# Optimization experiments

Hardware: AMD Instinct MI355X
Metric: run time of the kernel (lower is better)

The kernel has to match this reference:

```python
import jax, jax.numpy as jnp
import numpy as np

E, N, D_IN, HID, TD, H = 800000, 50000, 64, 32, 32, 4
HO = H * HID
VOCAB = 1000000


def time_encode(t, dim):
    # t: [E,1] -> [E,dim], interleaved sin/cos harmonic encoding
    div_term = jnp.exp(jnp.arange(0, dim, 2, dtype=jnp.float32) * (-jnp.log(10000.0) / dim))
    ang = t * div_term  # [E, dim//2]
    return jnp.stack([jnp.sin(ang), jnp.cos(ang)], axis=-1).reshape(t.shape[0], dim)


def tgat_conv(x, src, dst, t_feat, wq, bq, wk, bk, wv, bv, wt, bt, num_nodes):
    # x: [N, Fin]; t_feat: [E, TD]
    q = (x @ wq + bq).reshape(-1, H, HID)
    k = (x @ wk + bk).reshape(-1, H, HID)
    v = (x @ wv + bv).reshape(-1, H, HID)
    te = (t_feat @ wt + bt).reshape(-1, H, HID)
    q_i = q[dst]                      # [E,H,HID] gather at target
    k_j = k[src] + te                 # [E,H,HID] gather at source + time enc
    alpha = jnp.sum(q_i * k_j, axis=-1) / jnp.sqrt(jnp.float32(HID))  # [E,H]
    # segment softmax over edges grouped by destination node
    m = jax.ops.segment_max(alpha, dst, num_segments=num_nodes)        # [N,H]
    ex = jnp.exp(alpha - m[dst])
    s = jax.ops.segment_sum(ex, dst, num_segments=num_nodes)           # [N,H]
    a = ex / (s[dst] + 1e-16)                                          # [E,H]
    msg = v[src] * a[:, :, None]                                       # [E,H,HID]
    out = jax.ops.segment_sum(msg, dst, num_segments=num_nodes)        # [N,H,HID]
    return out.reshape(num_nodes, HO)


def setup_inputs() -> dict:
    key = jax.random.key(0)
    ks = jax.random.split(key, 24)

    def lin_w(k, fi, fo):
        return jax.random.normal(k, (fi, fo), dtype=jnp.float32) / jnp.sqrt(jnp.float32(fi))

    inp = {
        'edge_index': jax.random.randint(ks[0], (2, E), 0, N),
        'edge_attr': jax.random.uniform(ks[1], (E, 2), dtype=jnp.float32),
        'num_nodes': N,
        'emb': jax.random.normal(ks[2], (VOCAB, D_IN), dtype=jnp.float32) * 0.1,
        'wq1': lin_w(ks[3], D_IN, HO), 'bq1': jnp.zeros((HO,), jnp.float32),
        'wk1': lin_w(ks[4], D_IN, HO), 'bk1': jnp.zeros((HO,), jnp.float32),
        'wv1': lin_w(ks[5], D_IN, HO), 'bv1': jnp.zeros((HO,), jnp.float32),
        'wt1': lin_w(ks[6], TD, HO), 'bt1': jnp.zeros((HO,), jnp.float32),
        'wq2': lin_w(ks[7], HO, HO), 'bq2': jnp.zeros((HO,), jnp.float32),
        'wk2': lin_w(ks[8], HO, HO), 'bk2': jnp.zeros((HO,), jnp.float32),
        'wv2': lin_w(ks[9], HO, HO), 'bv2': jnp.zeros((HO,), jnp.float32),
        'wt2': lin_w(ks[10], TD, HO), 'bt2': jnp.zeros((HO,), jnp.float32),
        'wc': lin_w(ks[11], HO, 1), 'bc': jnp.zeros((1,), jnp.float32),
    }
    return inp


def reference(edge_index, edge_attr, num_nodes, emb,
              wq1, bq1, wk1, bk1, wv1, bv1, wt1, bt1,
              wq2, bq2, wk2, bk2, wv2, bv2, wt2, bt2,
              wc, bc):
    src, dst = edge_index[0], edge_index[1]
    x = emb[:num_nodes]                                   # node_emb(arange(N))
    raw_time = edge_attr[:, 1:2]                          # [E,1]
    t_feat = time_encode(raw_time, TD)                    # [E,TD]
    x = jax.nn.relu(tgat_conv(x, src, dst, t_feat, wq1, bq1, wk1, bk1, wv1, bv1, wt1, bt1, num_nodes))
    x = jax.nn.relu(tgat_conv(x, src, dst, t_feat, wq2, bq2, wk2, bk2, wv2, bv2, wt2, bt2, num_nodes))
    edge_emb = x[src] + x[dst]                            # [E,HO]
    return (edge_emb @ wc + bc).squeeze(-1)               # [E]
```

## Files before the change

### kernel.cpp

```cpp
#include <hip/hip_runtime.h>
#include <hip/hip_bf16.h>

#define NNODES 50000
#define HOUT   128
#define NHEAD  4
#define HID    32
#define TDIM   32

typedef _Float16 h8 __attribute__((ext_vector_type(8)));

__constant__ float DIVT[16] = {
    1.0f, 0.5623413251903491f, 0.31622776601683794f, 0.1778279410038923f,
    0.1f, 0.05623413251903491f, 0.03162277660168379f, 0.01778279410038923f,
    0.01f, 0.005623413251903491f, 0.003162277660168379f, 0.001778279410038923f,
    0.001f, 0.0005623413251903491f, 0.0003162277660168379f, 0.0001778279410038923f
};

__global__ __launch_bounds__(128) void prep_wqt_kernel(
    const float* __restrict__ wq, const float* __restrict__ bq,
    const float* __restrict__ wt, float* __restrict__ wqt,
    float* __restrict__ bqt, int din)
{
    __shared__ float wts[TDIM * HOUT];
    const int tid = threadIdx.x;
    for (int i = tid; i < TDIM * HOUT; i += 128) wts[i] = wt[i];
    __syncthreads();
    const int h = tid >> 5;
    const int t = tid & 31;
    const int d = blockIdx.x;
    const float* row = (d == din) ? bq : wq + (size_t)d * HOUT;
    float s = 0.f;
    #pragma unroll
    for (int d2 = 0; d2 < 32; d2++)
        s += row[h * 32 + d2] * wts[t * HOUT + h * 32 + d2];
    if (d == din) bqt[h * 32 + t] = s;
    else          wqt[(size_t)d * HOUT + h * 32 + t] = s;
}

__global__ __launch_bounds__(256) void gemm_qkv_kernel(
    const float* __restrict__ X, int din, int n,
    const float* __restrict__ W0, const float* __restrict__ W1,
    const float* __restrict__ W2, const float* __restrict__ W3,
    const float* __restrict__ B0, const float* __restrict__ B1,
    const float* __restrict__ B2, const float* __restrict__ B3,
    float* __restrict__ q, _Float16* __restrict__ kv, float* __restrict__ qwt)
{
    const int y = blockIdx.y;
    const float* W = (y == 0) ? W0 : (y == 1) ? W1 : (y == 2) ? W2 : W3;
    const float* B = (y == 0) ? B0 : (y == 1) ? B1 : (y == 2) ? B2 : B3;

    __shared__ float Xs[64 * 68];
    __shared__ float Ws[64 * HOUT];

    const int tid  = threadIdx.x;
    const int row0 = blockIdx.x * 64;
    const int rg   = tid >> 4;
    const int cg   = tid & 15;

    float acc[4][8];
    #pragma unroll
    for (int r = 0; r < 4; r++)
        #pragma unroll
        for (int c = 0; c < 8; c++) acc[r][c] = 0.f;

    const int ktiles = din >> 6;
    for (int kt = 0; kt < ktiles; kt++) {
        {
            const int lrow = tid >> 2;
            const int k0   = (tid & 3) << 4;
            const int grow = row0 + lrow;
            const float* src = X + (size_t)grow * din + kt * 64 + k0;
            #pragma unroll
            for (int i = 0; i < 4; i++) {
                float4 val = (grow < n) ? ((const float4*)src)[i]
                                        : make_float4(0.f, 0.f, 0.f, 0.f);
                *(float4*)&Xs[lrow * 68 + k0 + i * 4] = val;
            }
        }
        {
            const int k  = tid >> 2;
            const int c0 = (tid & 3) << 5;
            const float* src = W + (size_t)(kt * 64 + k) * HOUT + c0;
            #pragma unroll
            for (int i = 0; i < 8; i++)
                *(float4*)&Ws[k * HOUT + c0 + i * 4] = ((const float4*)src)[i];
        }
        __syncthreads();

        #pragma unroll 8
        for (int k = 0; k < 64; k++) {
            float4 b0 = *(const float4*)&Ws[k * HOUT + cg * 8];
            float4 b1 = *(const float4*)&Ws[k * HOUT + cg * 8 + 4];
            #pragma unroll
            for (int r = 0; r < 4; r++) {
                float a = Xs[(rg * 4 + r) * 68 + k];
                acc[r][0] += a * b0.x; acc[r][1] += a * b0.y;
                acc[r][2] += a * b0.z; acc[r][3] += a * b0.w;
                acc[r][4] += a * b1.x; acc[r][5] += a * b1.y;
                acc[r][6] += a * b1.z; acc[r][7] += a * b1.w;
            }
        }
        __syncthreads();
    }

    float4 bb0 = *(const float4*)&B[cg * 8];
    float4 bb1 = *(const float4*)&B[cg * 8 + 4];
    #pragma unroll
    for (int r = 0; r < 4; r++) {
        const int grow = row0 + rg * 4 + r;
        if (grow >= n) continue;
        float o[8] = {acc[r][0] + bb0.x, acc[r][1] + bb0.y, acc[r][2] + bb0.z,
                      acc[r][3] + bb0.w, acc[r][4] + bb1.x, acc[r][5] + bb1.y,
                      acc[r][6] + bb1.z, acc[r][7] + bb1.w};
        if (y == 0 || y == 3) {
            float* O = (y == 0) ? q : qwt;
            *(float4*)&O[(size_t)grow * HOUT + cg * 8]     = make_float4(o[0], o[1], o[2], o[3]);
            *(float4*)&O[(size_t)grow * HOUT + cg * 8 + 4] = make_float4(o[4], o[5], o[6], o[7]);
        } else {
            _Float16* O = kv + ((y == 1) ? 0 : 128);
            h8 hv;
            #pragma unroll
            for (int j = 0; j < 8; j++) hv[j] = (_Float16)o[j];
            *(h8*)&O[(size_t)grow * 256 + cg * 8] = hv;
        }
    }
}

__global__ __launch_bounds__(256) void hist_kernel(
    const int* __restrict__ ei, int* __restrict__ cnt, int E)
{
    const int e = blockIdx.x * 256 + threadIdx.x;
    if (e >= E) return;
    atomicAdd(&cnt[ei[E + e]], 1);
}

__global__ __launch_bounds__(1024) void scan_kernel(
    const int* __restrict__ cnt, int* __restrict__ off, int n)
{
    __shared__ int wsum[16];
    const int tid   = threadIdx.x;
    const int chunk = (n + 1023) >> 10;
    const int lo    = min(tid * chunk, n);
    const int hi    = min(lo + chunk, n);
    int s = 0;
    for (int i = lo; i < hi; i++) s += cnt[i];

    const int lane = tid & 63, wv = tid >> 6;
    int v = s;
    #pragma unroll
    for (int d = 1; d < 64; d <<= 1) {
        int t = __shfl_up(v, d);
        if (lane >= d) v += t;
    }
    if (lane == 63) wsum[wv] = v;
    __syncthreads();
    if (wv == 0 && lane < 16) {
        int w = wsum[lane];
        #pragma unroll
        for (int d = 1; d < 16; d <<= 1) {
            int t = __shfl_up(w, d);
            if (lane >= d) w += t;
        }
        wsum[lane] = w;
    }
    __syncthreads();
    int run = ((wv > 0) ? wsum[wv - 1] : 0) + (v - s);
    for (int i = lo; i < hi; i++) { off[i] = run; run += cnt[i]; }
    if (tid == 1023) off[n] = run;
}

__global__ __launch_bounds__(256) void scatter_kernel(
    const int* __restrict__ ei, const float* __restrict__ ea,
    const int* __restrict__ off, int* __restrict__ cur,
    int2* __restrict__ recs, int E)
{
    const int e = blockIdx.x * 256 + threadIdx.x;
    if (e >= E) return;
    const int dn = ei[E + e];
    const int pos = off[dn] + atomicAdd(&cur[dn], 1);
    recs[pos] = make_int2(ei[e], __float_as_int(ea[2 * e + 1]));
}

__global__ __launch_bounds__(256) void node_attn_kernel(
    const int* __restrict__ off, const int2* __restrict__ recs,
    const float* __restrict__ q, const _Float16* __restrict__ kv,
    const float* __restrict__ qwt, const float* __restrict__ bt,
    float* __restrict__ x, const float* __restrict__ wc,
    float* __restrict__ p, int n)
{
    const int wid = (blockIdx.x * 256 + threadIdx.x) >> 6;
    if (wid >= n) return;
    const int lane = threadIdx.x & 63;
    const int slot = lane >> 4;
    const int sub  = lane & 15;
    const int c0   = sub * 8;
    const int dn   = wid;

    const float4* qv = (const float4*)(q   + (size_t)dn * HOUT + c0);
    const float4* wv = (const float4*)(qwt + (size_t)dn * HOUT + c0);
    const float4 q0 = qv[0], q1 = qv[1];
    const float4 w0 = wv[0], w1 = wv[1];

    const float4 bt0 = ((const float4*)(bt + c0))[0];
    const float4 bt1 = ((const float4*)(bt + c0))[1];
    float qb = q0.x * bt0.x + q0.y * bt0.y + q0.z * bt0.z + q0.w * bt0.w +
               q1.x * bt1.x + q1.y * bt1.y + q1.z * bt1.z + q1.w * bt1.w;
    qb += __shfl_xor(qb, 1);
    qb += __shfl_xor(qb, 2);

    const int beg = off[dn];
    const int end = off[dn + 1];

    float acc[8] = {0.f, 0.f, 0.f, 0.f, 0.f, 0.f, 0.f, 0.f};
    float den = 0.f;

    for (int i = beg + slot; i < end; i += 4) {
        const int2 rec = recs[i];
        const int   sn = rec.x;
        const float rt = __int_as_float(rec.y);

        const h8 kk = *(const h8*)(kv + (size_t)sn * 256 + c0);
        const h8 vv = *(const h8*)(kv + (size_t)sn * 256 + 128 + c0);

        const int i0 = (sub & 3) * 4;
        float tf[8];
        #pragma unroll
        for (int jj = 0; jj < 4; jj++) {
            float s_, c_;
            __sincosf(rt * DIVT[i0 + jj], &s_, &c_);
            tf[2 * jj]     = s_;
            tf[2 * jj + 1] = c_;
        }

        float partial =
            q0.x * (float)kk[0] + q0.y * (float)kk[1] +
            q0.z * (float)kk[2] + q0.w * (float)kk[3] +
            q1.x * (float)kk[4] + q1.y * (float)kk[5] +
            q1.z * (float)kk[6] + q1.w * (float)kk[7] +
            w0.x * tf[0] + w0.y * tf[1] + w0.z * tf[2] + w0.w * tf[3] +
            w1.x * tf[4] + w1.y * tf[5] + w1.z * tf[6] + w1.w * tf[7];
        if ((sub & 3) == 0) partial += qb;

        partial += __shfl_xor(partial, 1);
        partial += __shfl_xor(partial, 2);

        const float ex = __expf(partial * 0.17677669529663687f);
        den += ex;
        #pragma unroll
        for (int j = 0; j < 8; j++) acc[j] += ex * (float)vv[j];
    }

    #pragma unroll
    for (int j = 0; j < 8; j++) {
        acc[j] += __shfl_xor(acc[j], 16);
        acc[j] += __shfl_xor(acc[j], 32);
    }
    den += __shfl_xor(den, 16);
    den += __shfl_xor(den, 32);

    if (lane < 16) {
        const float inv = 1.f / (den + 1e-16f);
        float o[8];
        #pragma unroll
        for (int j = 0; j < 8; j++) o[j] = fmaxf(acc[j] * inv, 0.f);
        if (p == nullptr) {
            float* xo = x + (size_t)dn * HOUT + c0;
            *(float4*)xo       = make_float4(o[0], o[1], o[2], o[3]);
            *((float4*)xo + 1) = make_float4(o[4], o[5], o[6], o[7]);
        } else {
            const float4 wc0 = ((const float4*)(wc + c0))[0];
            const float4 wc1 = ((const float4*)(wc + c0))[1];
            float pp = o[0] * wc0.x + o[1] * wc0.y + o[2] * wc0.z + o[3] * wc0.w +
                       o[4] * wc1.x + o[5] * wc1.y + o[6] * wc1.z + o[7] * wc1.w;
            pp += __shfl_xor(pp, 1);
            pp += __shfl_xor(pp, 2);
            pp += __shfl_xor(pp, 4);
            pp += __shfl_xor(pp, 8);
            if (sub == 0) p[dn] = pp;
        }
    }
}

__global__ __launch_bounds__(256) void edge_out_kernel(
    const int* __restrict__ ei, const float* __restrict__ p,
    const float* __restrict__ bc, float* __restrict__ out, int E)
{
    const int e = blockIdx.x * 256 + threadIdx.x;
    if (e >= E) return;
    out[e] = p[ei[e]] + p[ei[E + e]] + bc[0];
}

extern "C" void kernel_launch(void* const* d_in, const int* in_sizes, int n_in,
                              void* d_out, int out_size, void* d_ws, size_t ws_size,
                              hipStream_t stream)
{
    const int E = in_sizes[0] / 2;
    const int N = NNODES;

    const int*   ei  = (const int*)d_in[0];
    const float* ea  = (const float*)d_in[1];
    const float* emb = (const float*)d_in[3];
    const float *wq1 = (const float*)d_in[4],  *bq1 = (const float*)d_in[5];
    const float *wk1 = (const float*)d_in[6],  *bk1 = (const float*)d_in[7];
    const float *wv1 = (const float*)d_in[8],  *bv1 = (const float*)d_in[9];
    const float *wt1 = (const float*)d_in[10], *bt1 = (const float*)d_in[11];
    const float *wq2 = (const float*)d_in[12], *bq2 = (const float*)d_in[13];
    const float *wk2 = (const float*)d_in[14], *bk2 = (const float*)d_in[15];
    const float *wv2 = (const float*)d_in[16], *bv2 = (const float*)d_in[17];
    const float *wt2 = (const float*)d_in[18], *bt2 = (const float*)d_in[19];
    const float *wc  = (const float*)d_in[20], *bc  = (const float*)d_in[21];
    float* out = (float*)d_out;

    float* ws = (float*)d_ws;
    const size_t NF = (size_t)N * HOUT;
    float*     q    = ws;
    float*     qwt  = ws + NF;
    float*     xbuf = ws + 2 * NF;
    _Float16*  kv   = (_Float16*)(ws + 3 * NF);
    int2*      recs = (int2*)(ws + 4 * NF);
    float*     wqt1 = (float*)(recs + E);
    float*     wqt2 = wqt1 + 64 * HOUT;
    float*     bqt1 = wqt2 + 128 * HOUT;
    float*     bqt2 = bqt1 + HOUT;
    int*       cnt  = (int*)(bqt2 + HOUT);
    int*       off  = cnt + N;
    int*       cur  = off + N + 1;
    float*     p    = (float*)(cur + N);

    const dim3 ggemm((N + 63) / 64, 4);
    const int  eblk = (E + 255) / 256;
    const int  nblk = (N + 3) / 4;

    prep_wqt_kernel<<<65, 128, 0, stream>>>(wq1, bq1, wt1, wqt1, bqt1, 64);
    prep_wqt_kernel<<<129, 128, 0, stream>>>(wq2, bq2, wt2, wqt2, bqt2, 128);

    hipMemsetAsync(cnt, 0, (size_t)N * sizeof(int), stream);
    hipMemsetAsync(cur, 0, (size_t)N * sizeof(int), stream);
    hist_kernel<<<eblk, 256, 0, stream>>>(ei, cnt, E);
    scan_kernel<<<1, 1024, 0, stream>>>(cnt, off, N);
    scatter_kernel<<<eblk, 256, 0, stream>>>(ei, ea, off, cur, recs, E);

    gemm_qkv_kernel<<<ggemm, 256, 0, stream>>>(emb, 64, N,
        wq1, wk1, wv1, wqt1, bq1, bk1, bv1, bqt1, q, kv, qwt);
    node_attn_kernel<<<nblk, 256, 0, stream>>>(off, recs, q, kv, qwt, bt1,
                                               xbuf, nullptr, nullptr, N);

    gemm_qkv_kernel<<<ggemm, 256, 0, stream>>>(xbuf, 128, N,
        wq2, wk2, wv2, wqt2, bq2, bk2, bv2, bqt2, q, kv, qwt);
    node_attn_kernel<<<nblk, 256, 0, stream>>>(off, recs, q, kv, qwt, bt2,
                                               nullptr, wc, p, N);

    edge_out_kernel<<<(E + 255) / 256, 256, 0, stream>>>(ei, p, bc, out, E);
}
```

Before: 772.4 us.

## Use split-fp16 MFMA for QKV projection GEMM and parallelize offset scan

Replaces the scalar FP32 QKV GEMM with MFMA 16x16x32 f16 instructions. Inputs and weights are split into hi and lo halves (three MFMAs per tile) to keep near-FP32 accuracy, and a new prep kernel pre-splits and transposes the weights. Separately, the single-block serial CSR offset scan becomes a three-kernel multi-block scan over int4 chunks. These target the compute cost of the projection GEMMs and the serial scan latency. In exchange they add extra launches, more shared-memory traffic, and scalar (non-vectorized) output stores.

```diff
diff --git a/kernel.cpp b/kernel.cpp
--- a/kernel.cpp
+++ b/kernel.cpp
@@ -8,6 +8,8 @@
 #define TDIM   32
 
 typedef _Float16 h8 __attribute__((ext_vector_type(8)));
+typedef _Float16 h4 __attribute__((ext_vector_type(4)));
+typedef float    f4 __attribute__((ext_vector_type(4)));
 
 __constant__ float DIVT[16] = {
     1.0f, 0.5623413251903491f, 0.31622776601683794f, 0.1778279410038923f,
@@ -37,31 +39,53 @@
     else          wqt[(size_t)d * HOUT + h * 32 + t] = s;
 }
 
-__global__ __launch_bounds__(256) void gemm_qkv_kernel(
-    const float* __restrict__ X, int din, int n,
+__global__ void prep_wsplit_kernel(
     const float* __restrict__ W0, const float* __restrict__ W1,
     const float* __restrict__ W2, const float* __restrict__ W3,
+    _Float16* __restrict__ hi, _Float16* __restrict__ lo, int din)
+{
+    const int y = blockIdx.y, col = blockIdx.x, k = threadIdx.x;
+    const float* W = (y == 0) ? W0 : (y == 1) ? W1 : (y == 2) ? W2 : W3;
+    const float w = W[(size_t)k * HOUT + col];
+    const _Float16 h = (_Float16)w;
+    const size_t idx = ((size_t)y * HOUT + col) * din + k;
+    hi[idx] = h;
+    lo[idx] = (_Float16)(w - (float)h);
+}
+
+#define GPITCH 72
+
+__global__ __launch_bounds__(256) void gemm_qkv_mfma_kernel(
+    const float* __restrict__ X, int din, int n,
+    const _Float16* __restrict__ Whi, const _Float16* __restrict__ Wlo,
     const float* __restrict__ B0, const float* __restrict__ B1,
     const float* __restrict__ B2, const float* __restrict__ B3,
     float* __restrict__ q, _Float16* __restrict__ kv, float* __restrict__ qwt)
 {
     const int y = blockIdx.y;
-    const float* W = (y == 0) ? W0 : (y == 1) ? W1 : (y == 2) ? W2 : W3;
     const float* B = (y == 0) ? B0 : (y == 1) ? B1 : (y == 2) ? B2 : B3;
-
-    __shared__ float Xs[64 * 68];
-    __shared__ float Ws[64 * HOUT];
+    const _Float16* Wy_hi = Whi + (size_t)y * HOUT * din;
+    const _Float16* Wy_lo = Wlo + (size_t)y * HOUT * din;
+
+    __shared__ _Float16 Xh[64 * GPITCH];
+    __shared__ _Float16 Xl[64 * GPITCH];
+    __shared__ _Float16 Bh[128 * GPITCH];
+    __shared__ _Float16 Bl[128 * GPITCH];
 
     const int tid  = threadIdx.x;
     const int row0 = blockIdx.x * 64;
-    const int rg   = tid >> 4;
-    const int cg   = tid & 15;
-
-    float acc[4][8];
-    #pragma unroll
-    for (int r = 0; r < 4; r++)
-        #pragma unroll
-        for (int c = 0; c < 8; c++) acc[r][c] = 0.f;
+    const int wv   = tid >> 6;
+    const int lane = tid & 63;
+    const int lm   = lane & 15;
+    const int g    = lane >> 4;
+
+    f4 acc[8];
+    #pragma unroll
+    for (int ct = 0; ct < 8; ct++) acc[ct] = (f4){0.f, 0.f, 0.f, 0.f};
+
+    float bias[8];
+    #pragma unroll
+    for (int ct = 0; ct < 8; ct++) bias[ct] = B[ct * 16 + lm];
 
     const int ktiles = din >> 6;
     for (int kt = 0; kt < ktiles; kt++) {
@@ -72,56 +96,60 @@
             const float* src = X + (size_t)grow * din + kt * 64 + k0;
             #pragma unroll
             for (int i = 0; i < 4; i++) {
-                float4 val = (grow < n) ? ((const float4*)src)[i]
-                                        : make_float4(0.f, 0.f, 0.f, 0.f);
-                *(float4*)&Xs[lrow * 68 + k0 + i * 4] = val;
+                float4 v = (grow < n) ? ((const float4*)src)[i]
+                                      : make_float4(0.f, 0.f, 0.f, 0.f);
+                h4 hi, lo;
+                hi[0] = (_Float16)v.x; hi[1] = (_Float16)v.y;
+                hi[2] = (_Float16)v.z; hi[3] = (_Float16)v.w;
+                lo[0] = (_Float16)(v.x - (float)hi[0]);
+                lo[1] = (_Float16)(v.y - (float)hi[1]);
+                lo[2] = (_Float16)(v.z - (float)hi[2]);
+                lo[3] = (_Float16)(v.w - (float)hi[3]);
+                *(h4*)&Xh[lrow * GPITCH + k0 + 4 * i] = hi;
+                *(h4*)&Xl[lrow * GPITCH + k0 + 4 * i] = lo;
             }
         }
         {
-            const int k  = tid >> 2;
-            const int c0 = (tid & 3) << 5;
-            const float* src = W + (size_t)(kt * 64 + k) * HOUT + c0;
+            const int col = tid >> 1;
+            const int kk0 = (tid & 1) << 5;
+            const _Float16* sh = Wy_hi + (size_t)col * din + kt * 64 + kk0;
+            const _Float16* sl = Wy_lo + (size_t)col * din + kt * 64 + kk0;
             #pragma unroll
-            for (int i = 0; i < 8; i++)
-                *(float4*)&Ws[k * HOUT + c0 + i * 4] = ((const float4*)src)[i];
+            for (int i = 0; i < 4; i++) {
+                *(h8*)&Bh[col * GPITCH + kk0 + 8 * i] = ((const h8*)sh)[i];
+                *(h8*)&Bl[col * GPITCH + kk0 + 8 * i] = ((const h8*)sl)[i];
+            }
         }
         __syncthreads();
 
-        #pragma unroll 8
-        for (int k = 0; k < 64; k++) {
-            float4 b0 = *(const float4*)&Ws[k * HOUT + cg * 8];
-            float4 b1 = *(const float4*)&Ws[k * HOUT + cg * 8 + 4];
+        #pragma unroll
+        for (int kc = 0; kc < 2; kc++) {
+            const int kb = kc * 32 + g * 8;
+            const h8 ah = *(const h8*)&Xh[(wv * 16 + lm) * GPITCH + kb];
+            const h8 al = *(const h8*)&Xl[(wv * 16 + lm) * GPITCH + kb];
             #pragma unroll
-            for (int r = 0; r < 4; r++) {
-                float a = Xs[(rg * 4 + r) * 68 + k];
-                acc[r][0] += a * b0.x; acc[r][1] += a * b0.y;
-                acc[r][2] += a * b0.z; acc[r][3] += a * b0.w;
-                acc[r][4] += a * b1.x; acc[r][5] += a * b1.y;
-                acc[r][6] += a * b1.z; acc[r][7] += a * b1.w;
+            for (int ct = 0; ct < 8; ct++) {
+                const h8 bh = *(const h8*)&Bh[(ct * 16 + lm) * GPITCH + kb];
+                const h8 bl = *(const h8*)&Bl[(ct * 16 + lm) * GPITCH + kb];
+                acc[ct] = __builtin_amdgcn_mfma_f32_16x16x32_f16(ah, bh, acc[ct], 0, 0, 0);
+                acc[ct] = __builtin_amdgcn_mfma_f32_16x16x32_f16(al, bh, acc[ct], 0, 0, 0);
+                acc[ct] = __builtin_amdgcn_mfma_f32_16x16x32_f16(ah, bl, acc[ct], 0, 0, 0);
             }
         }
         __syncthreads();
     }
 
-    float4 bb0 = *(const float4*)&B[cg * 8];
-    float4 bb1 = *(const float4*)&B[cg * 8 + 4];
-    #pragma unroll
-    for (int r = 0; r < 4; r++) {
-        const int grow = row0 + rg * 4 + r;
-        if (grow >= n) continue;
-        float o[8] = {acc[r][0] + bb0.x, acc[r][1] + bb0.y, acc[r][2] + bb0.z,
-                      acc[r][3] + bb0.w, acc[r][4] + bb1.x, acc[r][5] + bb1.y,
-                      acc[r][6] + bb1.z, acc[r][7] + bb1.w};
-        if (y == 0 || y == 3) {
-            float* O = (y == 0) ? q : qwt;
-            *(float4*)&O[(size_t)grow * HOUT + cg * 8]     = make_float4(o[0], o[1], o[2], o[3]);
-            *(float4*)&O[(size_t)grow * HOUT + cg * 8 + 4] = make_float4(o[4], o[5], o[6], o[7]);
-        } else {
-            _Float16* O = kv + ((y == 1) ? 0 : 128);
-            h8 hv;
-            #pragma unroll
-            for (int j = 0; j < 8; j++) hv[j] = (_Float16)o[j];
-            *(h8*)&O[(size_t)grow * 256 + cg * 8] = hv;
+    #pragma unroll
+    for (int ct = 0; ct < 8; ct++) {
+        const int col = ct * 16 + lm;
+        #pragma unroll
+        for (int r = 0; r < 4; r++) {
+            const int grow = row0 + wv * 16 + g * 4 + r;
+            if (grow >= n) continue;
+            const float o = acc[ct][r] + bias[ct];
+            if (y == 0)      q[(size_t)grow * HOUT + col] = o;
+            else if (y == 3) qwt[(size_t)grow * HOUT + col] = o;
+            else             kv[(size_t)grow * 256 + ((y == 1) ? 0 : 128) + col] = (_Float16)o;
         }
     }
 }
@@ -134,39 +162,61 @@
     atomicAdd(&cnt[ei[E + e]], 1);
 }
 
-__global__ __launch_bounds__(1024) void scan_kernel(
-    const int* __restrict__ cnt, int* __restrict__ off, int n)
-{
-    __shared__ int wsum[16];
-    const int tid   = threadIdx.x;
-    const int chunk = (n + 1023) >> 10;
-    const int lo    = min(tid * chunk, n);
-    const int hi    = min(lo + chunk, n);
+__global__ __launch_bounds__(256) void scan_sum_kernel(
+    const int* __restrict__ cnt, int* __restrict__ bsum, int n4)
+{
+    const int i = blockIdx.x * 256 + threadIdx.x;
     int s = 0;
-    for (int i = lo; i < hi; i++) s += cnt[i];
-
-    const int lane = tid & 63, wv = tid >> 6;
-    int v = s;
+    if (i < n4) { int4 c = ((const int4*)cnt)[i]; s = c.x + c.y + c.z + c.w; }
+    #pragma unroll
+    for (int d = 1; d < 64; d <<= 1) s += __shfl_xor(s, d);
+    __shared__ int wsum[4];
+    if ((threadIdx.x & 63) == 0) wsum[threadIdx.x >> 6] = s;
+    __syncthreads();
+    if (threadIdx.x == 0) bsum[blockIdx.x] = wsum[0] + wsum[1] + wsum[2] + wsum[3];
+}
+
+__global__ __launch_bounds__(64) void scan_top_kernel(
+    const int* __restrict__ bsum, int* __restrict__ bpre,
+    int* __restrict__ offN, int nb)
+{
+    const int t = threadIdx.x;
+    const int v = (t < nb) ? bsum[t] : 0;
+    int incl = v;
     #pragma unroll
     for (int d = 1; d < 64; d <<= 1) {
-        int t = __shfl_up(v, d);
-        if (lane >= d) v += t;
-    }
-    if (lane == 63) wsum[wv] = v;
+        int u = __shfl_up(incl, d);
+        if (t >= d) incl += u;
+    }
+    if (t < nb) bpre[t] = incl - v;
+    if (t == 63) offN[0] = incl;
+}
+
+__global__ __launch_bounds__(256) void scan_write_kernel(
+    const int* __restrict__ cnt, const int* __restrict__ bpre,
+    int* __restrict__ off, int n4)
+{
+    const int i = blockIdx.x * 256 + threadIdx.x;
+    int4 c = make_int4(0, 0, 0, 0);
+    if (i < n4) c = ((const int4*)cnt)[i];
+    const int s = c.x + c.y + c.z + c.w;
+    int incl = s;
+    const int lane = threadIdx.x & 63;
+    #pragma unroll
+    for (int d = 1; d < 64; d <<= 1) {
+        int u = __shfl_up(incl, d);
+        if (lane >= d) incl += u;
+    }
+    __shared__ int wsum[4];
+    const int wv = threadIdx.x >> 6;
+    if (lane == 63) wsum[wv] = incl;
     __syncthreads();
-    if (wv == 0 && lane < 16) {
-        int w = wsum[lane];
-        #pragma unroll
-        for (int d = 1; d < 16; d <<= 1) {
-            int t = __shfl_up(w, d);
-            if (lane >= d) w += t;
-        }
-        wsum[lane] = w;
-    }
-    __syncthreads();
-    int run = ((wv > 0) ? wsum[wv - 1] : 0) + (v - s);
-    for (int i = lo; i < hi; i++) { off[i] = run; run += cnt[i]; }
-    if (tid == 1023) off[n] = run;
+    int base = bpre[blockIdx.x];
+    for (int w = 0; w < wv; w++) base += wsum[w];
+    const int excl = base + incl - s;
+    if (i < n4)
+        ((int4*)off)[i] = make_int4(excl, excl + c.x, excl + c.x + c.y,
+                                    excl + c.x + c.y + c.z);
 }
 
 __global__ __launch_bounds__(256) void scatter_kernel(
@@ -322,31 +372,43 @@
     float*     wqt2 = wqt1 + 64 * HOUT;
     float*     bqt1 = wqt2 + 128 * HOUT;
     float*     bqt2 = bqt1 + HOUT;
-    int*       cnt  = (int*)(bqt2 + HOUT);
+    _Float16*  whi1 = (_Float16*)(bqt2 + HOUT);
+    _Float16*  wlo1 = whi1 + 4 * HOUT * 64;
+    _Float16*  whi2 = wlo1 + 4 * HOUT * 64;
+    _Float16*  wlo2 = whi2 + 4 * HOUT * 128;
+    int*       cnt  = (int*)(wlo2 + 4 * HOUT * 128);
     int*       off  = cnt + N;
     int*       cur  = off + N + 1;
     float*     p    = (float*)(cur + N);
+    int*       bsum = (int*)(p + N);
+    int*       bpre = bsum + 64;
 
     const dim3 ggemm((N + 63) / 64, 4);
-    const int  eblk = (E + 255) / 256;
-    const int  nblk = (N + 3) / 4;
+    const int  eblk  = (E + 255) / 256;
+    const int  nblk  = (N + 3) / 4;
+    const int  n4    = N / 4;
+    const int  sblk  = (n4 + 255) / 256;
 
     prep_wqt_kernel<<<65, 128, 0, stream>>>(wq1, bq1, wt1, wqt1, bqt1, 64);
     prep_wqt_kernel<<<129, 128, 0, stream>>>(wq2, bq2, wt2, wqt2, bqt2, 128);
+    prep_wsplit_kernel<<<dim3(HOUT, 4), 64, 0, stream>>>(wq1, wk1, wv1, wqt1, whi1, wlo1, 64);
+    prep_wsplit_kernel<<<dim3(HOUT, 4), 128, 0, stream>>>(wq2, wk2, wv2, wqt2, whi2, wlo2, 128);
 
     hipMemsetAsync(cnt, 0, (size_t)N * sizeof(int), stream);
     hipMemsetAsync(cur, 0, (size_t)N * sizeof(int), stream);
     hist_kernel<<<eblk, 256, 0, stream>>>(ei, cnt, E);
-    scan_kernel<<<1, 1024, 0, stream>>>(cnt, off, N);
+    scan_sum_kernel<<<sblk, 256, 0, stream>>>(cnt, bsum, n4);
+    scan_top_kernel<<<1, 64, 0, stream>>>(bsum, bpre, off + N, sblk);
+    scan_write_kernel<<<sblk, 256, 0, stream>>>(cnt, bpre, off, n4);
     scatter_kernel<<<eblk, 256, 0, stream>>>(ei, ea, off, cur, recs, E);
 
-    gemm_qkv_kernel<<<ggemm, 256, 0, stream>>>(emb, 64, N,
-        wq1, wk1, wv1, wqt1, bq1, bk1, bv1, bqt1, q, kv, qwt);
+    gemm_qkv_mfma_kernel<<<ggemm, 256, 0, stream>>>(emb, 64, N,
+        whi1, wlo1, bq1, bk1, bv1, bqt1, q, kv, qwt);
     node_attn_kernel<<<nblk, 256, 0, stream>>>(off, recs, q, kv, qwt, bt1,
                                                xbuf, nullptr, nullptr, N);
 
-    gemm_qkv_kernel<<<ggemm, 256, 0, stream>>>(xbuf, 128, N,
-        wq2, wk2, wv2, wqt2, bq2, bk2, bv2, bqt2, q, kv, qwt);
+    gemm_qkv_mfma_kernel<<<ggemm, 256, 0, stream>>>(xbuf, 128, N,
+        whi2, wlo2, bq2, bk2, bv2, bqt2, q, kv, qwt);
     node_attn_kernel<<<nblk, 256, 0, stream>>>(off, recs, q, kv, qwt, bt2,
                                                nullptr, wc, p, N);
 
```

After: 656.5 us. 1.18x faster.
